# Performance work log

Measured on AMD Instinct MI355X. Metric: run time of the kernel, lower is better.

The kernel has to match this reference:

```python
import jax, jax.numpy as jnp
import numpy as np

G = 32          # grid_size
H = 12          # num_heads
D = 768         # embed_dim
HD = D // H     # head_dim = 64
FF = 3072       # ff_dim
B, T = 2, 2048
SPAN = 2 * G - 1        # 63
SPAN_C = 4 * G + 1      # 129
EPS = 1e-5


def setup_inputs() -> dict:
    key = jax.random.key(0)
    ks = jax.random.split(key, 16)
    s = 0.02
    is_sep = jax.random.uniform(ks[6], (T,)) < 0.05
    demo_id = jax.random.randint(ks[5], (T,), 0, 8)
    demo_id = jnp.where(is_sep, -1, demo_id)
    return {
        'x': jax.random.normal(ks[0], (B, T, D), jnp.float32),
        'row': jax.random.randint(ks[1], (T,), 0, G),
        'col': jax.random.randint(ks[2], (T,), 0, G),
        'demo_row': jax.random.randint(ks[3], (T,), 0, G),
        'demo_col': jax.random.randint(ks[4], (T,), 0, 2 * G),
        'demo_id': demo_id,
        'is_sep': is_sep,
        'ln1_w': jnp.ones((D,), jnp.float32),
        'ln1_b': jnp.zeros((D,), jnp.float32),
        'ln2_w': jnp.ones((D,), jnp.float32),
        'ln2_b': jnp.zeros((D,), jnp.float32),
        'qkv_w': jax.random.normal(ks[7], (D, 3 * D), jnp.float32) * s,
        'qkv_b': jnp.zeros((3 * D,), jnp.float32),
        'proj_w': jax.random.normal(ks[8], (D, D), jnp.float32) * s,
        'proj_b': jnp.zeros((D,), jnp.float32),
        'ff1_w': jax.random.normal(ks[9], (D, FF), jnp.float32) * s,
        'ff1_b': jnp.zeros((FF,), jnp.float32),
        'ff2_w': jax.random.normal(ks[10], (FF, D), jnp.float32) * s,
        'ff2_b': jnp.zeros((D,), jnp.float32),
        'rel_emb': jax.random.normal(ks[11], (SPAN * SPAN, H), jnp.float32) * s,
        'demo_emb': jax.random.normal(ks[12], (SPAN_C * SPAN, H), jnp.float32) * s,
    }


def _ln(x, w, b):
    m = jnp.mean(x, -1, keepdims=True)
    v = jnp.mean((x - m) ** 2, -1, keepdims=True)
    return (x - m) / jnp.sqrt(v + EPS) * w + b


def _rel_bias(rel_emb, row, col, is_sep):
    g1 = G - 1
    dr = jnp.clip(row[:, None] - row[None, :], -g1, g1) + g1
    dc = jnp.clip(col[:, None] - col[None, :], -g1, g1) + g1
    bias = rel_emb[dr * SPAN + dc]              # (T, T, H)
    valid = ~is_sep
    vp = (valid[:, None] & valid[None, :]).astype(jnp.float32)
    return jnp.transpose(bias, (2, 0, 1)) * vp[None]  # (H, T, T)


def _demo_bias(demo_emb, drow, dcol, did, is_sep):
    g1 = G - 1
    dr = jnp.clip(drow[:, None] - drow[None, :], -g1, g1) + g1
    dc = jnp.clip(dcol[:, None] - dcol[None, :], -2 * G, 2 * G) + 2 * G
    bias = demo_emb[dr * SPAN_C + dc]           # (T, T, H)
    valid = ~is_sep
    same = (did[:, None] == did[None, :]) & (did[:, None] >= 0) & (did[None, :] >= 0)
    vp = (valid[:, None] & valid[None, :] & same).astype(jnp.float32)
    return jnp.transpose(bias, (2, 0, 1)) * vp[None]


def reference(x, row, col, demo_row, demo_col, demo_id, is_sep,
              ln1_w, ln1_b, ln2_w, ln2_b, qkv_w, qkv_b, proj_w, proj_b,
              ff1_w, ff1_b, ff2_w, ff2_b, rel_emb, demo_emb):
    b, t, d = x.shape
    h1 = _ln(x, ln1_w, ln1_b)
    qkv = h1 @ qkv_w + qkv_b                        # (B, T, 3D)
    q, k, v = jnp.split(qkv, 3, axis=-1)
    q = q.reshape(b, t, H, HD).transpose(0, 2, 1, 3)  # (B, H, T, HD)
    k = k.reshape(b, t, H, HD).transpose(0, 2, 1, 3)
    v = v.reshape(b, t, H, HD).transpose(0, 2, 1, 3)
    scale = float(HD) ** -0.5
    logits = jnp.einsum('bhqd,bhkd->bhqk', q, k) * scale
    bias = _rel_bias(rel_emb, row, col, is_sep) + _demo_bias(demo_emb, demo_row, demo_col, demo_id, is_sep)
    attn = jax.nn.softmax(logits + bias[None], axis=-1)
    out = jnp.einsum('bhqk,bhkd->bhqd', attn, v)
    out = out.transpose(0, 2, 1, 3).reshape(b, t, D)
    out = out @ proj_w + proj_b
    x = x + out
    h2 = _ln(x, ln2_w, ln2_b)
    ff = jax.nn.gelu(h2 @ ff1_w + ff1_b, approximate=False) @ ff2_w + ff2_b
    return x + ff
```

## Files before the change

### kernel.cpp

```cpp
#include <hip/hip_runtime.h>
#include <hip/hip_bf16.h>
#include <hip/hip_fp16.h>
#include <math.h>

#define G_ 32
#define H_ 12
#define D_ 768
#define HD_ 64
#define FF_ 3072
#define B_ 2
#define T_ 2048
#define SPAN_ 63
#define SPANC_ 129
#define EPSF 1e-5f

typedef short bf16x8 __attribute__((ext_vector_type(8)));
typedef short short4v __attribute__((ext_vector_type(4)));
typedef float f32x4 __attribute__((ext_vector_type(4)));

__device__ __forceinline__ short f2bf(float f) {
    unsigned u = __builtin_bit_cast(unsigned, f);
    u = u + 0x7FFFu + ((u >> 16) & 1u);
    return (short)(u >> 16);
}

__device__ __forceinline__ unsigned char f2e5m2(float f) {
    unsigned short u = __half_as_ushort(__float2half(f));
    u = (unsigned short)(u + 0x7F + ((u >> 8) & 1));
    return (unsigned char)(u >> 8);
}
__device__ __forceinline__ float e5m2f(unsigned u) {
    return __half2float(__ushort_as_half((unsigned short)(u << 8)));
}

__device__ __forceinline__ void gl_lds16(const void* g, void* l) {
    __builtin_amdgcn_global_load_lds(
        (const __attribute__((address_space(1))) unsigned int*)g,
        (__attribute__((address_space(3))) unsigned int*)l, 16, 0, 0);
}

__global__ __launch_bounds__(256) void ln_bf16_kernel(const float* __restrict__ x,
                                                      const float* __restrict__ w,
                                                      const float* __restrict__ b,
                                                      short* __restrict__ out) {
    int wv = threadIdx.x >> 6;
    int lane = threadIdx.x & 63;
    int rowi = blockIdx.x * 4 + wv;
    const float* xr = x + (size_t)rowi * D_;
    float vals[12];
    float s = 0.f;
#pragma unroll
    for (int i = 0; i < 12; ++i) { vals[i] = xr[lane + i * 64]; s += vals[i]; }
#pragma unroll
    for (int off = 32; off > 0; off >>= 1) s += __shfl_xor(s, off, 64);
    float mean = s * (1.0f / D_);
    float vs = 0.f;
#pragma unroll
    for (int i = 0; i < 12; ++i) { float d = vals[i] - mean; vs += d * d; }
#pragma unroll
    for (int off = 32; off > 0; off >>= 1) vs += __shfl_xor(vs, off, 64);
    float rstd = rsqrtf(vs * (1.0f / D_) + EPSF);
    short* outr = out + (size_t)rowi * D_;
#pragma unroll
    for (int i = 0; i < 12; ++i) {
        int c = lane + i * 64;
        outr[c] = f2bf((vals[i] - mean) * rstd * w[c] + b[c]);
    }
}

__global__ __launch_bounds__(256) void tcast_kernel(const float* __restrict__ W,
                                                    short* __restrict__ Wt,
                                                    int K, int N) {
    __shared__ float t[32][33];
    int n0 = blockIdx.x * 32, k0 = blockIdx.y * 32;
    int tid = threadIdx.x;
    int r = tid >> 3, c4 = (tid & 7) * 4;
    float4 v = *(const float4*)(W + (size_t)(k0 + r) * N + n0 + c4);
    t[r][c4 + 0] = v.x; t[r][c4 + 1] = v.y; t[r][c4 + 2] = v.z; t[r][c4 + 3] = v.w;
    __syncthreads();
    short4v o;
    o[0] = f2bf(t[c4 + 0][r]); o[1] = f2bf(t[c4 + 1][r]);
    o[2] = f2bf(t[c4 + 2][r]); o[3] = f2bf(t[c4 + 3][r]);
    *(short4v*)(Wt + (size_t)(n0 + r) * K + k0 + c4) = o;
}

__global__ __launch_bounds__(256) void bias_build(
    const int* __restrict__ rowp, const int* __restrict__ colp,
    const int* __restrict__ drowp, const int* __restrict__ dcolp,
    const int* __restrict__ didp,
    const float* __restrict__ rel_emb, const float* __restrict__ demo_emb,
    unsigned char* __restrict__ biasT) {
    __shared__ unsigned char patch[12][16][80];
    int k0 = blockIdx.x * 64, q0 = blockIdx.y * 16;
    int tid = threadIdx.x;
    int qi = tid >> 4, kq = (tid & 15) * 4;
    int q = q0 + qi;
    int idq = didp[q];
    int rq = rowp[q], cq = colp[q], drq = drowp[q], dcq = dcolp[q];
    float bvs[4][12];
#pragma unroll
    for (int j = 0; j < 4; ++j) {
        int k = k0 + kq + j;
        int idk = didp[k];
        float4 v0 = {0.f, 0.f, 0.f, 0.f}, v1 = v0, v2 = v0;
        if (idq >= 0 && idk >= 0) {
            int dr = min(max(rq - rowp[k], -(G_ - 1)), G_ - 1) + (G_ - 1);
            int dc = min(max(cq - colp[k], -(G_ - 1)), G_ - 1) + (G_ - 1);
            const float* rp = rel_emb + (size_t)(dr * SPAN_ + dc) * 12;
            v0 = *(const float4*)rp;
            v1 = *(const float4*)(rp + 4);
            v2 = *(const float4*)(rp + 8);
            if (idq == idk) {
                int ddr = min(max(drq - drowp[k], -(G_ - 1)), G_ - 1) + (G_ - 1);
                int ddc = min(max(dcq - dcolp[k], -2 * G_), 2 * G_) + 2 * G_;
                const float* dp = demo_emb + (size_t)(ddr * SPANC_ + ddc) * 12;
                float4 w0 = *(const float4*)dp;
                float4 w1 = *(const float4*)(dp + 4);
                float4 w2 = *(const float4*)(dp + 8);
                v0.x += w0.x; v0.y += w0.y; v0.z += w0.z; v0.w += w0.w;
                v1.x += w1.x; v1.y += w1.y; v1.z += w1.z; v1.w += w1.w;
                v2.x += w2.x; v2.y += w2.y; v2.z += w2.z; v2.w += w2.w;
            }
        }
        bvs[j][0] = v0.x; bvs[j][1] = v0.y; bvs[j][2] = v0.z; bvs[j][3] = v0.w;
        bvs[j][4] = v1.x; bvs[j][5] = v1.y; bvs[j][6] = v1.z; bvs[j][7] = v1.w;
        bvs[j][8] = v2.x; bvs[j][9] = v2.y; bvs[j][10] = v2.z; bvs[j][11] = v2.w;
    }
#pragma unroll
    for (int h = 0; h < 12; ++h) {
        uchar4 pk;
        pk.x = f2e5m2(bvs[0][h]); pk.y = f2e5m2(bvs[1][h]);
        pk.z = f2e5m2(bvs[2][h]); pk.w = f2e5m2(bvs[3][h]);
        *(uchar4*)&patch[h][qi][kq] = pk;
    }
    __syncthreads();
    for (int c = tid; c < 768; c += 256) {
        int rowid = c >> 2, off = (c & 3) * 16;
        int h = rowid >> 4, q2 = rowid & 15;
        *(uint4*)(biasT + (size_t)h * T_ * T_ + (size_t)(q0 + q2) * T_ + k0 + off) =
            *(const uint4*)&patch[h][q2][off];
    }
}

enum { EPI_NONE = 0, EPI_RES = 1, EPI_GELU = 2 };

template <int EPI, int BF16OUT, int BM>
__global__ __launch_bounds__(256, 2) void gemm_bf16(const short* __restrict__ A,
                                                    const short* __restrict__ Bt,
                                                    const float* __restrict__ bias,
                                                    const float* __restrict__ res,
                                                    void* __restrict__ Cv,
                                                    int M, int N, int K) {
    __shared__ short As[BM * 64];
    __shared__ short Bs[128 * 64];
    constexpr int WM = BM / 2;
    constexpr int MF = WM / 16;
    int tid = threadIdx.x;
    int l = tid & 63;
    int w = tid >> 6;
    int wm = w >> 1, wn = w & 1;
    int row0 = blockIdx.y * BM, col0 = blockIdx.x * 128;
    int g = l >> 4, c16 = l & 15;
    f32x4 zero = {0.f, 0.f, 0.f, 0.f};
    f32x4 acc[MF][4];
#pragma unroll
    for (int m = 0; m < MF; ++m)
#pragma unroll
        for (int n = 0; n < 4; ++n) acc[m][n] = zero;

    int srowA = w * (BM / 4) + (l >> 3);
    int srowB = w * 32 + (l >> 3);
    int sseg0 = (l & 7);

    for (int k0 = 0; k0 < K; k0 += 64) {
#pragma unroll
        for (int inst = 0; inst < BM / 32; ++inst) {
            int arow = srowA + inst * 8;
            int seg = sseg0 ^ (arow & 7);
            gl_lds16(A + (size_t)(row0 + arow) * K + k0 + seg * 8,
                     &As[(w * (BM / 4) + inst * 8) * 64]);
        }
#pragma unroll
        for (int inst = 0; inst < 4; ++inst) {
            int brow = srowB + inst * 8;
            int seg = sseg0 ^ (brow & 7);
            gl_lds16(Bt + (size_t)(col0 + brow) * K + k0 + seg * 8,
                     &Bs[(w * 32 + inst * 8) * 64]);
        }
        __syncthreads();
#pragma unroll
        for (int dk = 0; dk < 2; ++dk) {
            bf16x8 af[MF], bfr[4];
#pragma unroll
            for (int m = 0; m < MF; ++m) {
                int r = wm * WM + m * 16 + c16;
                af[m] = *(const bf16x8*)&As[r * 64 + (((dk * 4 + g) ^ (r & 7)) << 3)];
            }
#pragma unroll
            for (int n = 0; n < 4; ++n) {
                int r = wn * 64 + n * 16 + c16;
                bfr[n] = *(const bf16x8*)&Bs[r * 64 + (((dk * 4 + g) ^ (r & 7)) << 3)];
            }
#pragma unroll
            for (int m = 0; m < MF; ++m)
#pragma unroll
                for (int n = 0; n < 4; ++n)
                    acc[m][n] = __builtin_amdgcn_mfma_f32_16x16x32_bf16(af[m], bfr[n], acc[m][n], 0, 0, 0);
        }
        __syncthreads();
    }

#pragma unroll
    for (int m = 0; m < MF; ++m)
#pragma unroll
        for (int n = 0; n < 4; ++n) {
            int rrow = row0 + wm * WM + m * 16 + g * 4;
            int ccol = col0 + wn * 64 + n * 16 + c16;
            float bv = bias[ccol];
#pragma unroll
            for (int i = 0; i < 4; ++i) {
                float v = acc[m][n][i] + bv;
                if (EPI == EPI_GELU) v = 0.5f * v * (1.f + erff(v * 0.70710678118f));
                if (EPI == EPI_RES) v += res[(size_t)(rrow + i) * N + ccol];
                if (BF16OUT)
                    ((short*)Cv)[(size_t)(rrow + i) * N + ccol] = f2bf(v);
                else
                    ((float*)Cv)[(size_t)(rrow + i) * N + ccol] = v;
            }
        }
}

__global__ __launch_bounds__(256, 2) void attn_mfma(
    const short* __restrict__ qkv,
    const unsigned char* __restrict__ biasT,
    short* __restrict__ attn_o) {
    __shared__ short Ks[2][64 * 64];
    __shared__ short Vt[2][64 * 72];
    __shared__ short Pb[4][16 * 72];

    int tid = threadIdx.x, w = tid >> 6, l = tid & 63;
    int g = l >> 4, c16 = l & 15;
    int bid = blockIdx.x;
    int nb = (bid & 7) * 96 + (bid >> 3);
    int qt = nb & 31, bh = nb >> 5;
    int h = bh % H_, b = bh / H_;
    int q0 = qt * 64;
    const int QS = 3 * D_;
    const short* kvbase = qkv + (size_t)b * T_ * QS;

    bf16x8 qf[2];
    {
        int qrow = q0 + w * 16 + c16;
        const short* qp = kvbase + (size_t)qrow * QS + h * HD_;
        qf[0] = *(const bf16x8*)(qp + g * 8);
        qf[1] = *(const bf16x8*)(qp + 32 + g * 8);
    }
    const unsigned char* bptr[4];
#pragma unroll
    for (int i = 0; i < 4; ++i)
        bptr[i] = biasT + (size_t)h * T_ * T_ + (size_t)(q0 + w * 16 + g * 4 + i) * T_;

    int krow = tid >> 3, kseg = tid & 7;
    int kx = (kseg ^ (krow & 7)) << 3;
    const short* kgp = kvbase + D_ + h * HD_ + kseg * 8;
    int vk0 = (tid & 31) * 2, vd0 = (tid >> 5) * 8;
    int vbase = ((((vk0 >> 3) ^ (vd0 >> 3)) & 7) << 3) + (vk0 & 7);
    const short* vgp = kvbase + 2 * D_ + h * HD_ + vd0;

    f32x4 zero = {0.f, 0.f, 0.f, 0.f};
    f32x4 oacc[4];
#pragma unroll
    for (int nf = 0; nf < 4; ++nf) oacc[nf] = zero;
    float lsum[4] = {0.f, 0.f, 0.f, 0.f};

    bf16x8 kr0, kr1, vr0, vr1;
    kr0 = *(const bf16x8*)(kgp + (size_t)krow * QS);
    kr1 = *(const bf16x8*)(kgp + (size_t)(krow + 32) * QS);
    vr0 = *(const bf16x8*)(vgp + (size_t)vk0 * QS);
    vr1 = *(const bf16x8*)(vgp + (size_t)(vk0 + 1) * QS);
    *(bf16x8*)&Ks[0][krow * 64 + kx] = kr0;
    *(bf16x8*)&Ks[0][(krow + 32) * 64 + kx] = kr1;
#pragma unroll
    for (int j = 0; j < 8; ++j) {
        unsigned pr = (unsigned)(ushort)vr0[j] | ((unsigned)(ushort)vr1[j] << 16);
        *(unsigned*)&Vt[0][(vd0 + j) * 72 + vbase] = pr;
    }
    {
        const short* kg1 = kgp + (size_t)64 * QS;
        const short* vg1 = vgp + (size_t)64 * QS;
        kr0 = *(const bf16x8*)(kg1 + (size_t)krow * QS);
        kr1 = *(const bf16x8*)(kg1 + (size_t)(krow + 32) * QS);
        vr0 = *(const bf16x8*)(vg1 + (size_t)vk0 * QS);
        vr1 = *(const bf16x8*)(vg1 + (size_t)(vk0 + 1) * QS);
    }

    for (int t = 0; t < 32; ++t) {
        __syncthreads();
        const short* KsC = Ks[t & 1];
        const short* VtC = Vt[t & 1];
        short* KsN = Ks[(t + 1) & 1];
        short* VtN = Vt[(t + 1) & 1];
        *(bf16x8*)&KsN[krow * 64 + kx] = kr0;
        *(bf16x8*)&KsN[(krow + 32) * 64 + kx] = kr1;
#pragma unroll
        for (int j = 0; j < 8; ++j) {
            unsigned pr = (unsigned)(ushort)vr0[j] | ((unsigned)(ushort)vr1[j] << 16);
            *(unsigned*)&VtN[(vd0 + j) * 72 + vbase] = pr;
        }
        {
            int kb2 = ((t + 2) & 31) * 64;
            const short* kg2 = kgp + (size_t)kb2 * QS;
            const short* vg2 = vgp + (size_t)kb2 * QS;
            kr0 = *(const bf16x8*)(kg2 + (size_t)krow * QS);
            kr1 = *(const bf16x8*)(kg2 + (size_t)(krow + 32) * QS);
            vr0 = *(const bf16x8*)(vg2 + (size_t)vk0 * QS);
            vr1 = *(const bf16x8*)(vg2 + (size_t)(vk0 + 1) * QS);
        }
        int kb = t * 64;
        float bv[16];
#pragma unroll
        for (int nf = 0; nf < 4; ++nf)
#pragma unroll
            for (int i = 0; i < 4; ++i)
                bv[nf * 4 + i] = e5m2f(bptr[i][kb + nf * 16 + c16]);
        f32x4 sac[4];
#pragma unroll
        for (int nf = 0; nf < 4; ++nf) sac[nf] = zero;
#pragma unroll
        for (int dk = 0; dk < 2; ++dk) {
#pragma unroll
            for (int nf = 0; nf < 4; ++nf) {
                int r = nf * 16 + c16;
                bf16x8 kf = *(const bf16x8*)&KsC[r * 64 + (((dk * 4 + g) ^ (r & 7)) << 3)];
                sac[nf] = __builtin_amdgcn_mfma_f32_16x16x32_bf16(qf[dk], kf, sac[nf], 0, 0, 0);
            }
        }
#pragma unroll
        for (int nf = 0; nf < 4; ++nf)
#pragma unroll
            for (int i = 0; i < 4; ++i) {
                float e = __expf(fmaf(sac[nf][i], 0.125f, bv[nf * 4 + i]));
                sac[nf][i] = e;
                lsum[i] += e;
            }
        short* pbw = &Pb[w][0];
#pragma unroll
        for (int nf = 0; nf < 4; ++nf) {
            int chunkbase = nf * 2 + (c16 >> 3);
            int kpos = c16 & 7;
#pragma unroll
            for (int i = 0; i < 4; ++i)
                pbw[(g * 4 + i) * 72 + (((chunkbase ^ g) & 7) << 3) + kpos] = f2bf(sac[nf][i]);
        }
#pragma unroll
        for (int dk = 0; dk < 2; ++dk) {
            bf16x8 pa = *(const bf16x8*)&pbw[c16 * 72 + (((dk * 4 + g) ^ (c16 >> 2)) & 7) * 8];
#pragma unroll
            for (int nf = 0; nf < 4; ++nf) {
                int d = nf * 16 + c16;
                bf16x8 vb = *(const bf16x8*)&VtC[d * 72 + (((dk * 4 + g) ^ (d >> 3)) & 7) * 8];
                oacc[nf] = __builtin_amdgcn_mfma_f32_16x16x32_bf16(pa, vb, oacc[nf], 0, 0, 0);
            }
        }
    }

#pragma unroll
    for (int i = 0; i < 4; ++i) {
#pragma unroll
        for (int off = 1; off < 16; off <<= 1) lsum[i] += __shfl_xor(lsum[i], off, 64);
    }

#pragma unroll
    for (int nf = 0; nf < 4; ++nf)
#pragma unroll
        for (int i = 0; i < 4; ++i) {
            float o = oacc[nf][i] / lsum[i];
            int qq = q0 + w * 16 + g * 4 + i;
            attn_o[(size_t)(b * T_ + qq) * D_ + h * HD_ + nf * 16 + c16] = f2bf(o);
        }
}

extern "C" void kernel_launch(void* const* d_in, const int* in_sizes, int n_in,
                              void* d_out, int out_size, void* d_ws, size_t ws_size,
                              hipStream_t stream) {
    const float* x = (const float*)d_in[0];
    const int* rowp = (const int*)d_in[1];
    const int* colp = (const int*)d_in[2];
    const int* drowp = (const int*)d_in[3];
    const int* dcolp = (const int*)d_in[4];
    const int* didp = (const int*)d_in[5];
    const float* ln1_w = (const float*)d_in[7];
    const float* ln1_b = (const float*)d_in[8];
    const float* ln2_w = (const float*)d_in[9];
    const float* ln2_b = (const float*)d_in[10];
    const float* qkv_w = (const float*)d_in[11];
    const float* qkv_b = (const float*)d_in[12];
    const float* proj_w = (const float*)d_in[13];
    const float* proj_b = (const float*)d_in[14];
    const float* ff1_w = (const float*)d_in[15];
    const float* ff1_b = (const float*)d_in[16];
    const float* ff2_w = (const float*)d_in[17];
    const float* ff2_b = (const float*)d_in[18];
    const float* rel_emb = (const float*)d_in[19];
    const float* demo_emb = (const float*)d_in[20];
    float* out = (float*)d_out;

    const int M = B_ * T_;
    char* p = (char*)d_ws;
    short* h1 = (short*)p;     p += (size_t)M * D_ * 2;
    short* qkvb = (short*)p;   p += (size_t)M * 3 * D_ * 2;
    short* attn_o = (short*)p; p += (size_t)M * D_ * 2;
    short* qkvt = (short*)p;   p += (size_t)(3 * D_) * D_ * 2;
    short* projt = (short*)p;  p += (size_t)D_ * D_ * 2;
    short* ff1t = (short*)p;   p += (size_t)FF_ * D_ * 2;
    short* ff2t = (short*)p;   p += (size_t)D_ * FF_ * 2;
    float* x2 = (float*)p;
    short* h2 = (short*)(p + (size_t)M * D_ * 4);
    short* ffact = (short*)(p + (size_t)M * D_ * 4 + (size_t)M * D_ * 2);
    unsigned char* biasT = (unsigned char*)p;

    bias_build<<<dim3(T_ / 64, T_ / 16), 256, 0, stream>>>(
        rowp, colp, drowp, dcolp, didp, rel_emb, demo_emb, biasT);
    tcast_kernel<<<dim3(3 * D_ / 32, D_ / 32), 256, 0, stream>>>(qkv_w, qkvt, D_, 3 * D_);
    tcast_kernel<<<dim3(D_ / 32, D_ / 32), 256, 0, stream>>>(proj_w, projt, D_, D_);
    tcast_kernel<<<dim3(FF_ / 32, D_ / 32), 256, 0, stream>>>(ff1_w, ff1t, D_, FF_);
    tcast_kernel<<<dim3(D_ / 32, FF_ / 32), 256, 0, stream>>>(ff2_w, ff2t, FF_, D_);

    ln_bf16_kernel<<<dim3(M / 4), 256, 0, stream>>>(x, ln1_w, ln1_b, h1);

    gemm_bf16<EPI_NONE, 1, 128><<<dim3(3 * D_ / 128, M / 128), 256, 0, stream>>>(
        h1, qkvt, qkv_b, nullptr, qkvb, M, 3 * D_, D_);

    attn_mfma<<<dim3(B_ * H_ * (T_ / 64)), 256, 0, stream>>>(qkvb, biasT, attn_o);

    gemm_bf16<EPI_RES, 0, 64><<<dim3(D_ / 128, M / 64), 256, 0, stream>>>(
        attn_o, projt, proj_b, x, x2, M, D_, D_);

    ln_bf16_kernel<<<dim3(M / 4), 256, 0, stream>>>(x2, ln2_w, ln2_b, h2);

    gemm_bf16<EPI_GELU, 1, 128><<<dim3(FF_ / 128, M / 128), 256, 0, stream>>>(
        h2, ff1t, ff1_b, nullptr, ffact, M, FF_, D_);

    gemm_bf16<EPI_RES, 0, 64><<<dim3(D_ / 128, M / 64), 256, 0, stream>>>(
        ffact, ff2t, ff2_b, x2, out, M, D_, FF_);
}
```

Measured before the change: 242.9 us.

## Transpose QK MFMA, vectorize bias loads and P stores, merge weight casts

```diff
diff --git a/kernel.cpp b/kernel.cpp
--- a/kernel.cpp
+++ b/kernel.cpp
@@ -68,11 +68,25 @@
     }
 }
 
-__global__ __launch_bounds__(256) void tcast_kernel(const float* __restrict__ W,
-                                                    short* __restrict__ Wt,
-                                                    int K, int N) {
+__global__ __launch_bounds__(256) void tcast_all(const float* __restrict__ qkv_w,
+                                                 const float* __restrict__ proj_w,
+                                                 const float* __restrict__ ff1_w,
+                                                 const float* __restrict__ ff2_w,
+                                                 short* __restrict__ qkvt,
+                                                 short* __restrict__ projt,
+                                                 short* __restrict__ ff1t,
+                                                 short* __restrict__ ff2t) {
     __shared__ float t[32][33];
-    int n0 = blockIdx.x * 32, k0 = blockIdx.y * 32;
+    int bid = blockIdx.x;
+    const float* W;
+    short* Wt;
+    int K, N, bx, lo;
+    if (bid < 1728)      { W = qkv_w;  Wt = qkvt;  K = D_;  N = 3 * D_; bx = 72; lo = 0; }
+    else if (bid < 2304) { W = proj_w; Wt = projt; K = D_;  N = D_;     bx = 24; lo = 1728; }
+    else if (bid < 4608) { W = ff1_w;  Wt = ff1t;  K = D_;  N = FF_;    bx = 96; lo = 2304; }
+    else                 { W = ff2_w;  Wt = ff2t;  K = FF_; N = D_;     bx = 24; lo = 4608; }
+    int rblk = bid - lo;
+    int n0 = (rblk % bx) * 32, k0 = (rblk / bx) * 32;
     int tid = threadIdx.x;
     int r = tid >> 3, c4 = (tid & 7) * 4;
     float4 v = *(const float4*)(W + (size_t)(k0 + r) * N + n0 + c4);
@@ -230,7 +244,7 @@
         }
 }
 
-__global__ __launch_bounds__(256, 2) void attn_mfma(
+__global__ __launch_bounds__(256, 3) void attn_mfma(
     const short* __restrict__ qkv,
     const unsigned char* __restrict__ biasT,
     short* __restrict__ attn_o) {
@@ -255,10 +269,8 @@
         qf[0] = *(const bf16x8*)(qp + g * 8);
         qf[1] = *(const bf16x8*)(qp + 32 + g * 8);
     }
-    const unsigned char* bptr[4];
-#pragma unroll
-    for (int i = 0; i < 4; ++i)
-        bptr[i] = biasT + (size_t)h * T_ * T_ + (size_t)(q0 + w * 16 + g * 4 + i) * T_;
+    const unsigned char* bq =
+        biasT + (size_t)h * T_ * T_ + (size_t)(q0 + w * 16 + c16) * T_;
 
     int krow = tid >> 3, kseg = tid & 7;
     int kx = (kseg ^ (krow & 7)) << 3;
@@ -271,7 +283,7 @@
     f32x4 oacc[4];
 #pragma unroll
     for (int nf = 0; nf < 4; ++nf) oacc[nf] = zero;
-    float lsum[4] = {0.f, 0.f, 0.f, 0.f};
+    float lsum = 0.f;
 
     bf16x8 kr0, kr1, vr0, vr1;
     kr0 = *(const bf16x8*)(kgp + (size_t)krow * QS);
@@ -317,12 +329,10 @@
             vr1 = *(const bf16x8*)(vg2 + (size_t)(vk0 + 1) * QS);
         }
         int kb = t * 64;
-        float bv[16];
+        uchar4 bu[4];
 #pragma unroll
         for (int nf = 0; nf < 4; ++nf)
-#pragma unroll
-            for (int i = 0; i < 4; ++i)
-                bv[nf * 4 + i] = e5m2f(bptr[i][kb + nf * 16 + c16]);
+            bu[nf] = *(const uchar4*)(bq + kb + nf * 16 + g * 4);
         f32x4 sac[4];
 #pragma unroll
         for (int nf = 0; nf < 4; ++nf) sac[nf] = zero;
@@ -332,25 +342,27 @@
             for (int nf = 0; nf < 4; ++nf) {
                 int r = nf * 16 + c16;
                 bf16x8 kf = *(const bf16x8*)&KsC[r * 64 + (((dk * 4 + g) ^ (r & 7)) << 3)];
-                sac[nf] = __builtin_amdgcn_mfma_f32_16x16x32_bf16(qf[dk], kf, sac[nf], 0, 0, 0);
-            }
-        }
-#pragma unroll
-        for (int nf = 0; nf < 4; ++nf)
-#pragma unroll
-            for (int i = 0; i < 4; ++i) {
-                float e = __expf(fmaf(sac[nf][i], 0.125f, bv[nf * 4 + i]));
-                sac[nf][i] = e;
-                lsum[i] += e;
-            }
+                sac[nf] = __builtin_amdgcn_mfma_f32_16x16x32_bf16(kf, qf[dk], sac[nf], 0, 0, 0);
+            }
+        }
+#pragma unroll
+        for (int nf = 0; nf < 4; ++nf) {
+            float e0 = __expf(fmaf(sac[nf][0], 0.125f, e5m2f(bu[nf].x)));
+            float e1 = __expf(fmaf(sac[nf][1], 0.125f, e5m2f(bu[nf].y)));
+            float e2 = __expf(fmaf(sac[nf][2], 0.125f, e5m2f(bu[nf].z)));
+            float e3 = __expf(fmaf(sac[nf][3], 0.125f, e5m2f(bu[nf].w)));
+            sac[nf][0] = e0; sac[nf][1] = e1; sac[nf][2] = e2; sac[nf][3] = e3;
+            lsum += (e0 + e1) + (e2 + e3);
+        }
         short* pbw = &Pb[w][0];
 #pragma unroll
         for (int nf = 0; nf < 4; ++nf) {
-            int chunkbase = nf * 2 + (c16 >> 3);
-            int kpos = c16 & 7;
-#pragma unroll
-            for (int i = 0; i < 4; ++i)
-                pbw[(g * 4 + i) * 72 + (((chunkbase ^ g) & 7) << 3) + kpos] = f2bf(sac[nf][i]);
+            int chunk = nf * 2 + (g >> 1);
+            int slot = (chunk ^ (c16 >> 2)) & 7;
+            short4v pk;
+            pk[0] = f2bf(sac[nf][0]); pk[1] = f2bf(sac[nf][1]);
+            pk[2] = f2bf(sac[nf][2]); pk[3] = f2bf(sac[nf][3]);
+            *(short4v*)&pbw[c16 * 72 + slot * 8 + (g & 1) * 4] = pk;
         }
 #pragma unroll
         for (int dk = 0; dk < 2; ++dk) {
@@ -364,17 +376,15 @@
         }
     }
 
-#pragma unroll
-    for (int i = 0; i < 4; ++i) {
-#pragma unroll
-        for (int off = 1; off < 16; off <<= 1) lsum[i] += __shfl_xor(lsum[i], off, 64);
-    }
+    lsum += __shfl_xor(lsum, 16, 64);
+    lsum += __shfl_xor(lsum, 32, 64);
 
 #pragma unroll
     for (int nf = 0; nf < 4; ++nf)
 #pragma unroll
         for (int i = 0; i < 4; ++i) {
-            float o = oacc[nf][i] / lsum[i];
+            float denom = __shfl(lsum, g * 4 + i, 16);
+            float o = oacc[nf][i] / denom;
             int qq = q0 + w * 16 + g * 4 + i;
             attn_o[(size_t)(b * T_ + qq) * D_ + h * HD_ + nf * 16 + c16] = f2bf(o);
         }
@@ -421,10 +431,8 @@
 
     bias_build<<<dim3(T_ / 64, T_ / 16), 256, 0, stream>>>(
         rowp, colp, drowp, dcolp, didp, rel_emb, demo_emb, biasT);
-    tcast_kernel<<<dim3(3 * D_ / 32, D_ / 32), 256, 0, stream>>>(qkv_w, qkvt, D_, 3 * D_);
-    tcast_kernel<<<dim3(D_ / 32, D_ / 32), 256, 0, stream>>>(proj_w, projt, D_, D_);
-    tcast_kernel<<<dim3(FF_ / 32, D_ / 32), 256, 0, stream>>>(ff1_w, ff1t, D_, FF_);
-    tcast_kernel<<<dim3(D_ / 32, FF_ / 32), 256, 0, stream>>>(ff2_w, ff2t, FF_, D_);
+    tcast_all<<<dim3(6912), 256, 0, stream>>>(qkv_w, proj_w, ff1_w, ff2_w,
+                                              qkvt, projt, ff1t, ff2t);
 
     ln_bf16_kernel<<<dim3(M / 4), 256, 0, stream>>>(x, ln1_w, ln1_b, h1);
 
```

New measurement: 251.5 us. 1.04x slower.
